# Kernel tuning notes

Measured on AMD Instinct MI355X. Metric: run time of the kernel, lower is better.

## Reference

```python
import jax, jax.numpy as jnp
import numpy as np

NL, DM, DI, DS, DC, DR, NC = 4, 128, 256, 16, 4, 8, 10
ALPHA = 0.3  # observer_alpha

def layernorm(x, w, b, eps=1e-5):
    m = x.mean(-1, keepdims=True)
    v = ((x - m) ** 2).mean(-1, keepdims=True)
    return (x - m) / jnp.sqrt(v + eps) * w + b

def silu(x):
    return x * jax.nn.sigmoid(x)

def causal_dwconv(x, w, b):
    # x: (B, L, DI); w: (DI, 1, DC); b: (DI,)
    xt = x.transpose(0, 2, 1)  # (B, DI, L)
    y = jax.lax.conv_general_dilated(
        xt, w, window_strides=(1,), padding=[(DC - 1, 0)],
        dimension_numbers=('NCH', 'OIH', 'NCH'), feature_group_count=DI)
    return (y + b[None, :, None]).transpose(0, 2, 1)  # (B, L, DI)

def ssm_scan(delta, Bc, Cc, u, A):
    # delta, u: (B, L, DI); Bc, Cc: (B, L, DS); A: (DI, DS)
    B = delta.shape[0]
    def step(h, inp):
        d_t, b_t, c_t, u_t = inp  # (B,DI),(B,DS),(B,DS),(B,DI)
        dA = jnp.exp(d_t[..., None] * A)              # (B, DI, DS)
        h = dA * h + (d_t * u_t)[..., None] * b_t[:, None, :]
        y = jnp.einsum('bds,bs->bd', h, c_t)
        return h, y
    h0 = jnp.zeros((B, DI, DS), delta.dtype)
    xs = (delta.transpose(1, 0, 2), Bc.transpose(1, 0, 2),
          Cc.transpose(1, 0, 2), u.transpose(1, 0, 2))
    _, ys = jax.lax.scan(step, h0, xs)
    return ys.transpose(1, 0, 2)  # (B, L, DI)

def _forward(x, W_in, b_in, ln_w, ln_b, in_proj_w, conv_w, conv_b, x_proj_w,
             dt_proj_w, dt_proj_b, A_log, Dp, out_proj_w, out_proj_b,
             norm_w, norm_b, cls_w, cls_b):
    B = x.shape[0]
    u = x.transpose(0, 2, 3, 1).reshape(B, -1, 3)   # (B, L, 3)
    h = u @ W_in + b_in                              # (B, L, DM)
    for i in range(NL):
        res = h
        z = layernorm(h, ln_w[i], ln_b[i])
        xz = z @ in_proj_w[i]                        # (B, L, 2*DI)
        xin, gate = jnp.split(xz, 2, axis=-1)
        xc = silu(causal_dwconv(xin, conv_w[i], conv_b[i]))  # (B, L, DI)
        proj = xc @ x_proj_w[i]                      # (B, L, DR + 2*DS)
        dt, Bc, Cc = jnp.split(proj, [DR, DR + DS], axis=-1)
        delta = jax.nn.softplus(dt @ dt_proj_w[i] + dt_proj_b[i])  # (B, L, DI)
        A = -jnp.exp(A_log[i])                       # (DI, DS)
        y = ssm_scan(delta, Bc, Cc, xc, A) + xc * Dp[i]
        # Luenberger-style observer correction: blend predicted SSM output
        y = (1.0 - ALPHA) * y + ALPHA * xc
        y = y * silu(gate)
        h = res + y @ out_proj_w[i] + out_proj_b[i]
    pooled = h.mean(axis=1)                          # (B, DM)
    pooled = layernorm(pooled, norm_w, norm_b)
    return pooled @ cls_w + cls_b                    # (B, NC)

def setup_inputs():
    key = jax.random.key(0)
    ks = jax.random.split(key, 8)
    def nrm(k, shape, std=0.02):
        return jax.random.normal(k, shape, jnp.float32) * std
    return {
        'x': jax.random.normal(ks[0], (32, 3, 32, 32), jnp.float32),
        'W_in': nrm(ks[1], (3, DM)), 'b_in': jnp.zeros((DM,), jnp.float32),
        'ln_w': jnp.ones((NL, DM), jnp.float32), 'ln_b': jnp.zeros((NL, DM), jnp.float32),
        'in_proj_w': nrm(ks[2], (NL, DM, 2 * DI)),
        'conv_w': nrm(ks[3], (NL, DI, 1, DC), 0.2), 'conv_b': jnp.zeros((NL, DI), jnp.float32),
        'x_proj_w': nrm(ks[4], (NL, DI, DR + 2 * DS)),
        'dt_proj_w': nrm(ks[5], (NL, DR, DI), 0.1),
        'dt_proj_b': jnp.full((NL, DI), -4.6, jnp.float32),
        'A_log': jnp.log(jnp.broadcast_to(jnp.arange(1, DS + 1, dtype=jnp.float32), (NL, DI, DS))),
        'Dp': jnp.ones((NL, DI), jnp.float32),
        'out_proj_w': nrm(ks[6], (NL, DI, DM)), 'out_proj_b': jnp.zeros((NL, DM), jnp.float32),
        'norm_w': jnp.ones((DM,), jnp.float32), 'norm_b': jnp.zeros((DM,), jnp.float32),
        'cls_w': nrm(ks[7], (DM, NC)), 'cls_b': jnp.zeros((NC,), jnp.float32),
    }

def reference(x, W_in, b_in, ln_w, ln_b, in_proj_w, conv_w, conv_b, x_proj_w,
              dt_proj_w, dt_proj_b, A_log, Dp, out_proj_w, out_proj_b,
              norm_w, norm_b, cls_w, cls_b):
    return _forward(x, W_in, b_in, ln_w, ln_b, in_proj_w, conv_w, conv_b,
                    x_proj_w, dt_proj_w, dt_proj_b, A_log, Dp, out_proj_w,
                    out_proj_b, norm_w, norm_b, cls_w, cls_b)
```

## Files before the change

kernel.cpp:

```cpp
#include <hip/hip_runtime.h>
#include <math.h>

#define B_  32
#define L_  1024
#define T_  (B_ * L_)
#define DM_ 128
#define DI_ 256
#define DS_ 16
#define DC_ 4
#define DR_ 8
#define NC_ 10
#define CHUNK_ 64
#define NCH_  (L_ / CHUNK_)
#define PSTR_ 288

typedef __bf16 bf16x8 __attribute__((ext_vector_type(8)));
typedef __bf16 bf16x4 __attribute__((ext_vector_type(4)));
typedef __bf16 bf16x2 __attribute__((ext_vector_type(2)));
typedef float f32x4 __attribute__((ext_vector_type(4)));
typedef unsigned short u16x8 __attribute__((ext_vector_type(8)));

__device__ __forceinline__ float sigmoidf_(float x) { return 1.0f / (1.0f + __expf(-x)); }
__device__ __forceinline__ float siluf_(float x)    { return x * sigmoidf_(x); }
__device__ __forceinline__ float softplusf_(float x) {
    return (x > 15.0f) ? x : __logf(1.0f + __expf(x));
}
__device__ __forceinline__ float fexp2_(float x) { return __builtin_amdgcn_exp2f(x); }

__device__ __forceinline__ void gload_lds16(const __bf16* g, __bf16* l) {
    __builtin_amdgcn_global_load_lds(
        (const __attribute__((address_space(1))) void*)g,
        (__attribute__((address_space(3))) void*)l, 16, 0, 0);
}

template<int R>
__device__ __forceinline__ void stage_async(const __bf16* __restrict__ src,
        __bf16* lds, int k0, int stride, int wid, int lane) {
    constexpr int NI = R / 32;
#pragma unroll
    for (int j = 0; j < NI; ++j) {
        int s0 = (wid * NI + j) * 64;
        int s = s0 + lane;
        int row = s >> 3, sw = s & 7;
        int slot = sw ^ (row & 7);
        gload_lds16(src + (size_t)row * stride + k0 + slot * 8, lds + (size_t)s0 * 8);
    }
}

__global__ __launch_bounds__(128) void k_embed(const float* __restrict__ x,
        const float* __restrict__ Win, const float* __restrict__ bin,
        float* __restrict__ h) {
    int t = blockIdx.x;
    int b = t >> 10, l = t & 1023;
    int m = threadIdx.x;
    const float* xb = x + (size_t)b * 3 * 1024 + l;
    float acc = bin[m];
    acc = fmaf(xb[0],    Win[m],        acc);
    acc = fmaf(xb[1024], Win[128 + m],  acc);
    acc = fmaf(xb[2048], Win[256 + m],  acc);
    h[(size_t)t * 128 + m] = acc;
}

__global__ __launch_bounds__(256) void k_prep(const float* __restrict__ ipw,
        const float* __restrict__ opw, const float* __restrict__ xpw,
        const float* __restrict__ dtw, __bf16* __restrict__ wt1,
        __bf16* __restrict__ wt2, __bf16* __restrict__ wcat) {
    int blk = blockIdx.x;
    int tid = threadIdx.x;
    int i = blk * 256 + tid;
    if (i < 262144) {
        int lay = i >> 16, rem = i & 65535, n = rem >> 7, k = rem & 127;
        wt1[i] = (__bf16)ipw[lay * 65536 + k * 512 + n];
    }
    if (i < 131072) {
        int lay = i >> 15, rem = i & 32767, n = rem >> 8, k = rem & 255;
        wt2[i] = (__bf16)opw[lay * 32768 + k * 128 + n];
    }
    {
        int lay = blk / 384, n = blk % 384;
        int k = tid;
        float v;
        if (n < 256) {
            float acc = 0.0f;
#pragma unroll
            for (int r = 0; r < 8; ++r)
                acc = fmaf(xpw[lay * 10240 + k * 40 + r], dtw[lay * 2048 + r * 256 + n], acc);
            v = acc;
        } else if (n < 288) {
            v = xpw[lay * 10240 + k * 40 + (n - 248)];
        } else {
            v = 0.0f;
        }
        wcat[(size_t)blk * 256 + k] = (__bf16)v;
    }
}

__global__ __launch_bounds__(256) void k_ln(const float* __restrict__ h,
        const float* __restrict__ w, const float* __restrict__ b,
        __bf16* __restrict__ z) {
    int wid = threadIdx.x >> 6, lane = threadIdx.x & 63;
    int t = blockIdx.x * 4 + wid;
    const float* hr = h + (size_t)t * 128;
    float2 v = *(const float2*)(hr + lane * 2);
    float s = v.x + v.y, sq = v.x * v.x + v.y * v.y;
#pragma unroll
    for (int off = 1; off < 64; off <<= 1) {
        s += __shfl_xor(s, off);
        sq += __shfl_xor(sq, off);
    }
    float mean = s * (1.0f / 128.0f);
    float var = sq * (1.0f / 128.0f) - mean * mean;
    float rstd = rsqrtf(var + 1e-5f);
    float2 wv = *(const float2*)(w + lane * 2);
    float2 bv = *(const float2*)(b + lane * 2);
    bf16x2 o;
    o.x = (__bf16)((v.x - mean) * rstd * wv.x + bv.x);
    o.y = (__bf16)((v.y - mean) * rstd * wv.y + bv.y);
    *(bf16x2*)(z + (size_t)t * 128 + lane * 2) = o;
}

template<int BM, int K, int N, int MODE, bool GATE, bool WLN>
__global__ __launch_bounds__(256) void k_gemm_mfma(
        const __bf16* __restrict__ A, const __bf16* __restrict__ G,
        const __bf16* __restrict__ Wt, const float* __restrict__ bias,
        float* __restrict__ Cf, __bf16* __restrict__ Cb,
        const float* __restrict__ lnw, const float* __restrict__ lnb,
        __bf16* __restrict__ Zb) {
    static_assert(!GATE || BM == 32, "GATE staging assumes BM=32");
    static_assert(!WLN || (MODE == 2 && BM == 32 && N == 128), "WLN geometry");
    __shared__ __bf16 As[BM * 64];
    __shared__ __bf16 Bs[128 * 64];
    __shared__ float red_s[WLN ? 4 : 1][WLN ? 32 : 1];
    __shared__ float red_q[WLN ? 4 : 1][WLN ? 32 : 1];
    int tid = threadIdx.x;
    int bm = blockIdx.x, bn = blockIdx.y;
    int lane = tid & 63, wid = tid >> 6;
    int lr = lane & 15, lg = lane >> 4;
    constexpr int MF = BM / 16;

    f32x4 acc[MF][2] = {};
    const __bf16* Asrc = A + (size_t)(bm * BM) * K;
    const __bf16* Bsrc = Wt + (size_t)(bn * 128) * K;

    for (int k0 = 0; k0 < K; k0 += 64) {
        if (GATE) {
            int row = tid >> 3, slot = tid & 7;
            int m = bm * BM + row;
            bf16x8 yv = *(const bf16x8*)(A + (size_t)m * K + k0 + slot * 8);
            bf16x8 gv = *(const bf16x8*)(G + (size_t)m * 512 + 256 + k0 + slot * 8);
            bf16x8 v;
#pragma unroll
            for (int j = 0; j < 8; ++j)
                v[j] = (__bf16)((float)yv[j] * siluf_((float)gv[j]));
            *(bf16x8*)(As + row * 64 + ((slot ^ (row & 7)) * 8)) = v;
        } else {
            stage_async<BM>(Asrc, As, k0, K, wid, lane);
        }
        stage_async<128>(Bsrc, Bs, k0, K, wid, lane);
        __syncthreads();
#pragma unroll
        for (int ks = 0; ks < 2; ++ks) {
            int slotbase = ks * 4 + lg;
            bf16x8 af[MF], bfr[2];
#pragma unroll
            for (int m = 0; m < MF; ++m) {
                int row = m * 16 + lr;
                af[m] = *(const bf16x8*)(As + row * 64 + ((slotbase ^ (row & 7)) * 8));
            }
#pragma unroll
            for (int n = 0; n < 2; ++n) {
                int rn = wid * 32 + n * 16 + lr;
                bfr[n] = *(const bf16x8*)(Bs + rn * 64 + ((slotbase ^ (rn & 7)) * 8));
            }
#pragma unroll
            for (int m = 0; m < MF; ++m)
#pragma unroll
                for (int n = 0; n < 2; ++n)
                    acc[m][n] = __builtin_amdgcn_mfma_f32_16x16x32_bf16(
                        af[m], bfr[n], acc[m][n], 0, 0, 0);
        }
        __syncthreads();
    }
    float vv[MF][2][4];
#pragma unroll
    for (int m = 0; m < MF; ++m) {
#pragma unroll
        for (int n = 0; n < 2; ++n) {
            int col = bn * 128 + wid * 32 + n * 16 + lr;
            float bv = (MODE == 2) ? bias[col] : 0.0f;
            float dtbv = (MODE == 1 && col < 256) ? bias[col] : 0.0f;
#pragma unroll
            for (int rg = 0; rg < 4; ++rg) {
                int row = bm * BM + m * 16 + lg * 4 + rg;
                float v = acc[m][n][rg];
                if (MODE == 0) {
                    Cb[(size_t)row * N + col] = (__bf16)v;
                } else if (MODE == 1) {
                    if (col < 256)
                        Cb[(size_t)row * PSTR_ + col] = (__bf16)softplusf_(v + dtbv);
                    else if (col < 288)
                        Cb[(size_t)row * PSTR_ + col] = (__bf16)v;
                } else {
                    float* cp = Cf + (size_t)row * N + col;
                    v += *cp + bv;
                    *cp = v;
                    vv[m][n][rg] = v;
                }
            }
        }
    }
    if (WLN) {
        float ps[MF][4], pq[MF][4];
#pragma unroll
        for (int m = 0; m < MF; ++m)
#pragma unroll
            for (int rg = 0; rg < 4; ++rg) {
                float a = vv[m][0][rg], bv2 = vv[m][1][rg];
                ps[m][rg] = a + bv2;
                pq[m][rg] = a * a + bv2 * bv2;
            }
#pragma unroll
        for (int off = 1; off < 16; off <<= 1) {
#pragma unroll
            for (int m = 0; m < MF; ++m)
#pragma unroll
                for (int rg = 0; rg < 4; ++rg) {
                    ps[m][rg] += __shfl_xor(ps[m][rg], off);
                    pq[m][rg] += __shfl_xor(pq[m][rg], off);
                }
        }
        if (lr == 0) {
#pragma unroll
            for (int m = 0; m < MF; ++m)
#pragma unroll
                for (int rg = 0; rg < 4; ++rg) {
                    int rl = m * 16 + lg * 4 + rg;
                    red_s[wid][rl] = ps[m][rg];
                    red_q[wid][rl] = pq[m][rg];
                }
        }
        __syncthreads();
#pragma unroll
        for (int m = 0; m < MF; ++m)
#pragma unroll
            for (int rg = 0; rg < 4; ++rg) {
                int rl = m * 16 + lg * 4 + rg;
                float s = red_s[0][rl] + red_s[1][rl] + red_s[2][rl] + red_s[3][rl];
                float q = red_q[0][rl] + red_q[1][rl] + red_q[2][rl] + red_q[3][rl];
                float mean = s * (1.0f / 128.0f);
                float var = q * (1.0f / 128.0f) - mean * mean;
                float rstd = rsqrtf(var + 1e-5f);
#pragma unroll
                for (int n = 0; n < 2; ++n) {
                    int col = wid * 32 + n * 16 + lr;
                    float z = (vv[m][n][rg] - mean) * rstd * lnw[col] + lnb[col];
                    Zb[(size_t)(bm * BM + rl) * 128 + col] = (__bf16)z;
                }
            }
    }
}

__global__ __launch_bounds__(256) void k_conv(const __bf16* __restrict__ xzb,
        const float* __restrict__ cw, const float* __restrict__ cb,
        __bf16* __restrict__ xcb) {
    int t = blockIdx.x * 4 + (threadIdx.x >> 6);
    int d0 = (threadIdx.x & 63) * 4;
    int l = t & 1023;
    const __bf16* xp = xzb + (size_t)t * 512 + d0;
    float4 wv[4];
#pragma unroll
    for (int j = 0; j < 4; ++j) wv[j] = *(const float4*)(cw + (d0 + j) * 4);
    float acc[4] = {cb[d0], cb[d0 + 1], cb[d0 + 2], cb[d0 + 3]};
#pragma unroll
    for (int k = 0; k < 4; ++k) {
        int back = 3 - k;
        if (l >= back) {
            bf16x4 v = *(const bf16x4*)(xp - back * 512);
#pragma unroll
            for (int j = 0; j < 4; ++j)
                acc[j] = fmaf((float)v[j], ((const float*)&wv[j])[k], acc[j]);
        }
    }
    bf16x4 o;
#pragma unroll
    for (int j = 0; j < 4; ++j) o[j] = (__bf16)siluf_(acc[j]);
    *(bf16x4*)(xcb + (size_t)t * 256 + d0) = o;
}

template<bool FINAL>
__global__ __launch_bounds__(128) void k_scan_chunk(
        const __bf16* __restrict__ projall, const __bf16* __restrict__ xcb,
        const float* __restrict__ Alog, const float* __restrict__ Dp,
        float* __restrict__ P, float* __restrict__ S,
        __bf16* __restrict__ yb) {
    __shared__ unsigned du_lds[CHUNK_ * 128];
    __shared__ float bc[CHUNK_ * 32];
    int b = blockIdx.z, c = blockIdx.y, dg = blockIdx.x;
    int tid = threadIdx.x;
    int d = dg * 128 + tid;

    const __bf16* projC = projall + ((size_t)b * 1024 + c * CHUNK_) * PSTR_;
    const __bf16* xcC   = xcb + ((size_t)b * 1024 + c * CHUNK_) * 256 + dg * 128;

#pragma unroll
    for (int r = 0; r < 8; ++r) {
        int item = r * 128 + tid;
        int t = item >> 4, o8 = (item & 15) * 8;
        u16x8 dv = *(const u16x8*)(projC + (size_t)t * PSTR_ + dg * 128 + o8);
        u16x8 xv = *(const u16x8*)(xcC + (size_t)t * 256 + o8);
        uint4 w0, w1;
        w0.x = dv[0] | ((unsigned)xv[0] << 16); w0.y = dv[1] | ((unsigned)xv[1] << 16);
        w0.z = dv[2] | ((unsigned)xv[2] << 16); w0.w = dv[3] | ((unsigned)xv[3] << 16);
        w1.x = dv[4] | ((unsigned)xv[4] << 16); w1.y = dv[5] | ((unsigned)xv[5] << 16);
        w1.z = dv[6] | ((unsigned)xv[6] << 16); w1.w = dv[7] | ((unsigned)xv[7] << 16);
        *(uint4*)(du_lds + t * 128 + o8)     = w0;
        *(uint4*)(du_lds + t * 128 + o8 + 4) = w1;
    }
#pragma unroll
    for (int r = 0; r < 2; ++r) {
        int item = r * 128 + tid;
        int t = item >> 2, g8 = (item & 3) * 8;
        bf16x8 v = *(const bf16x8*)(projC + (size_t)t * PSTR_ + 256 + g8);
        float4 f0 = {(float)v[0], (float)v[1], (float)v[2], (float)v[3]};
        float4 f1 = {(float)v[4], (float)v[5], (float)v[6], (float)v[7]};
        *(float4*)(bc + t * 32 + g8)     = f0;
        *(float4*)(bc + t * 32 + g8 + 4) = f1;
    }

    float aa[16], hs[16];
#pragma unroll
    for (int jj = 0; jj < 4; ++jj) {
        float4 av = *(const float4*)(Alog + (size_t)d * 16 + jj * 4);
        aa[jj * 4 + 0] = -__expf(av.x) * 1.44269504088896f;
        aa[jj * 4 + 1] = -__expf(av.y) * 1.44269504088896f;
        aa[jj * 4 + 2] = -__expf(av.z) * 1.44269504088896f;
        aa[jj * 4 + 3] = -__expf(av.w) * 1.44269504088896f;
    }
    float Dpd = Dp[d];
    size_t psIdx = ((size_t)(b * NCH_ + c)) * 4096 + (size_t)d * 16;
#pragma unroll
    for (int j = 0; j < 16; ++j) hs[j] = 0.0f;
    if (FINAL) {
        for (int cc = 0; cc < c; ++cc) {
            size_t base = ((size_t)(b * NCH_ + cc)) * 4096 + (size_t)d * 16;
#pragma unroll
            for (int jj = 0; jj < 4; ++jj) {
                float4 p = *(const float4*)(P + base + jj * 4);
                float4 s = *(const float4*)(S + base + jj * 4);
                hs[jj * 4 + 0] = fmaf(p.x, hs[jj * 4 + 0], s.x);
                hs[jj * 4 + 1] = fmaf(p.y, hs[jj * 4 + 1], s.y);
                hs[jj * 4 + 2] = fmaf(p.z, hs[jj * 4 + 2], s.z);
                hs[jj * 4 + 3] = fmaf(p.w, hs[jj * 4 + 3], s.w);
            }
        }
    }
    float cumd = 0.0f;
    __bf16* yC = yb + ((size_t)b * 1024 + c * CHUNK_) * 256 + dg * 128 + tid;

    __syncthreads();
#pragma unroll 2
    for (int tt = 0; tt < CHUNK_; ++tt) {
        unsigned duv = du_lds[tt * 128 + tid];
        float delta_t = __uint_as_float(duv << 16);
        float u = __uint_as_float(duv & 0xffff0000u);
        float du = delta_t * u;
        const float* bcr = bc + tt * 32;
        if (!FINAL) cumd += delta_t;
        float ys = 0.0f;
#pragma unroll
        for (int jj = 0; jj < 4; ++jj) {
            float4 Bv = *(const float4*)(bcr + jj * 4);
            float4 Cv;
            if (FINAL) Cv = *(const float4*)(bcr + 16 + jj * 4);
#pragma unroll
            for (int j = 0; j < 4; ++j) {
                int s = jj * 4 + j;
                float dA = fexp2_(delta_t * aa[s]);
                hs[s] = fmaf(dA, hs[s], du * ((const float*)&Bv)[j]);
                if (FINAL) ys = fmaf(hs[s], ((const float*)&Cv)[j], ys);
            }
        }
        if (FINAL) {
            float yv = fmaf(u, Dpd, ys);
            yv = fmaf(0.7f, yv, 0.3f * u);
            yC[(size_t)tt * 256] = (__bf16)yv;
        }
    }
    if (!FINAL) {
#pragma unroll
        for (int jj = 0; jj < 4; ++jj) {
            float4 pv, sv;
            pv.x = fexp2_(aa[jj * 4 + 0] * cumd);
            pv.y = fexp2_(aa[jj * 4 + 1] * cumd);
            pv.z = fexp2_(aa[jj * 4 + 2] * cumd);
            pv.w = fexp2_(aa[jj * 4 + 3] * cumd);
            sv.x = hs[jj * 4 + 0]; sv.y = hs[jj * 4 + 1];
            sv.z = hs[jj * 4 + 2]; sv.w = hs[jj * 4 + 3];
            *(float4*)(P + psIdx + jj * 4) = pv;
            *(float4*)(S + psIdx + jj * 4) = sv;
        }
    }
}

__global__ __launch_bounds__(128) void k_pool(const float* __restrict__ h,
        float* __restrict__ partial) {
    int b = blockIdx.x, lc = blockIdx.y;
    int m = threadIdx.x;
    const float* hb = h + (size_t)b * 131072 + (size_t)lc * 128 * 128 + m;
    float acc = 0.0f;
#pragma unroll 8
    for (int l = 0; l < 128; ++l) acc += hb[(size_t)l * 128];
    partial[((size_t)b * 8 + lc) * 128 + m] = acc;
}

__global__ __launch_bounds__(128) void k_head(const float* __restrict__ partial,
        const float* __restrict__ nw, const float* __restrict__ nb,
        const float* __restrict__ cw, const float* __restrict__ cb,
        float* __restrict__ out) {
    __shared__ float zs[128];
    __shared__ float red[128];
    int b = blockIdx.x, m = threadIdx.x;
    float v = 0.0f;
#pragma unroll
    for (int lc = 0; lc < 8; ++lc) v += partial[((size_t)b * 8 + lc) * 128 + m];
    v *= (1.0f / 1024.0f);
    red[m] = v;
    __syncthreads();
    for (int off = 64; off; off >>= 1) {
        if (m < off) red[m] += red[m + off];
        __syncthreads();
    }
    float mean = red[0] * (1.0f / 128.0f);
    __syncthreads();
    float dv = v - mean;
    red[m] = dv * dv;
    __syncthreads();
    for (int off = 64; off; off >>= 1) {
        if (m < off) red[m] += red[m + off];
        __syncthreads();
    }
    float rstd = rsqrtf(red[0] * (1.0f / 128.0f) + 1e-5f);
    zs[m] = dv * rstd * nw[m] + nb[m];
    __syncthreads();
    if (m < NC_) {
        float acc = cb[m];
#pragma unroll 8
        for (int k = 0; k < 128; ++k) acc = fmaf(zs[k], cw[k * 10 + m], acc);
        out[b * 10 + m] = acc;
    }
}

extern "C" void kernel_launch(void* const* d_in, const int* in_sizes, int n_in,
                              void* d_out, int out_size, void* d_ws, size_t ws_size,
                              hipStream_t stream) {
    const float* x    = (const float*)d_in[0];
    const float* Win  = (const float*)d_in[1];
    const float* bin  = (const float*)d_in[2];
    const float* lnw  = (const float*)d_in[3];
    const float* lnb  = (const float*)d_in[4];
    const float* ipw  = (const float*)d_in[5];
    const float* cw   = (const float*)d_in[6];
    const float* cb   = (const float*)d_in[7];
    const float* xpw  = (const float*)d_in[8];
    const float* dtw  = (const float*)d_in[9];
    const float* dtb  = (const float*)d_in[10];
    const float* Alog = (const float*)d_in[11];
    const float* Dp   = (const float*)d_in[12];
    const float* opw  = (const float*)d_in[13];
    const float* opb  = (const float*)d_in[14];
    const float* nw   = (const float*)d_in[15];
    const float* nb   = (const float*)d_in[16];
    const float* clw  = (const float*)d_in[17];
    const float* clb  = (const float*)d_in[18];

    float* ws = (float*)d_ws;
    float*  h       = ws;
    float*  P       = ws + 4194304;
    float*  Sb      = ws + 6291456;
    __bf16* zb      = (__bf16*)P;
    __bf16* xzb     = (__bf16*)(ws + 8388608);
    __bf16* xcb     = (__bf16*)(ws + 16777216);
    __bf16* projall = (__bf16*)(ws + 20971520);
    __bf16* yb      = (__bf16*)(ws + 25690112);
    float*  partial = ws + 29884416;
    __bf16* wt1     = (__bf16*)(ws + 29917184);
    __bf16* wt2     = (__bf16*)(ws + 30048256);
    __bf16* wcat    = (__bf16*)(ws + 30113792);

    k_prep<<<1536, 256, 0, stream>>>(ipw, opw, xpw, dtw, wt1, wt2, wcat);
    k_embed<<<T_, 128, 0, stream>>>(x, Win, bin, h);
    k_ln<<<T_ / 4, 256, 0, stream>>>(h, lnw, lnb, zb);
    for (int lay = 0; lay < 4; ++lay) {
        k_gemm_mfma<64, 128, 512, 0, false, false><<<dim3(T_ / 64, 4), 256, 0, stream>>>(
            zb, nullptr, wt1 + (size_t)lay * 65536, nullptr, nullptr, xzb,
            nullptr, nullptr, nullptr);
        k_conv<<<T_ / 4, 256, 0, stream>>>(xzb, cw + lay * 1024, cb + lay * 256, xcb);
        k_gemm_mfma<64, 256, 384, 1, false, false><<<dim3(T_ / 64, 3), 256, 0, stream>>>(
            xcb, nullptr, wcat + (size_t)lay * 98304, dtb + lay * 256, nullptr, projall,
            nullptr, nullptr, nullptr);
        k_scan_chunk<false><<<dim3(2, NCH_, B_), 128, 0, stream>>>(projall, xcb,
            Alog + lay * 4096, Dp + lay * 256, P, Sb, yb);
        k_scan_chunk<true><<<dim3(2, NCH_, B_), 128, 0, stream>>>(projall, xcb,
            Alog + lay * 4096, Dp + lay * 256, P, Sb, yb);
        if (lay < 3) {
            k_gemm_mfma<32, 256, 128, 2, true, true><<<dim3(T_ / 32, 1), 256, 0, stream>>>(
                yb, xzb, wt2 + (size_t)lay * 32768, opb + lay * 128, h, nullptr,
                lnw + (lay + 1) * 128, lnb + (lay + 1) * 128, zb);
        } else {
            k_gemm_mfma<32, 256, 128, 2, true, false><<<dim3(T_ / 32, 1), 256, 0, stream>>>(
                yb, xzb, wt2 + (size_t)lay * 32768, opb + lay * 128, h, nullptr,
                nullptr, nullptr, nullptr);
        }
    }
    k_pool<<<dim3(32, 8), 128, 0, stream>>>(h, partial);
    k_head<<<32, 128, 0, stream>>>(partial, nw, nb, clw, clb, (float*)d_out);
}
```

Baseline: 642.7 us.

## Halve scan chunk size and add separate chunk-state combine kernel

Reduces the scan chunk length from 64 to 32, doubling the number of chunk blocks to raise parallelism in the two scan passes. The per-block serial prefix over earlier chunk states in the final pass is replaced by a dedicated combine kernel that computes each chunk's starting state once and writes it back into P. The S buffer is moved to a new workspace offset because P/S now span twice as many chunks, and one extra kernel launch per layer is added.

```diff
diff --git a/kernel.cpp b/kernel.cpp
--- a/kernel.cpp
+++ b/kernel.cpp
@@ -10,7 +10,7 @@
 #define DC_ 4
 #define DR_ 8
 #define NC_ 10
-#define CHUNK_ 64
+#define CHUNK_ 32
 #define NCH_  (L_ / CHUNK_)
 #define PSTR_ 288
 
@@ -303,7 +303,7 @@
     const __bf16* xcC   = xcb + ((size_t)b * 1024 + c * CHUNK_) * 256 + dg * 128;
 
 #pragma unroll
-    for (int r = 0; r < 8; ++r) {
+    for (int r = 0; r < (CHUNK_ * 16) / 128; ++r) {
         int item = r * 128 + tid;
         int t = item >> 4, o8 = (item & 15) * 8;
         u16x8 dv = *(const u16x8*)(projC + (size_t)t * PSTR_ + dg * 128 + o8);
@@ -317,7 +317,7 @@
         *(uint4*)(du_lds + t * 128 + o8 + 4) = w1;
     }
 #pragma unroll
-    for (int r = 0; r < 2; ++r) {
+    for (int r = 0; r < (CHUNK_ * 4) / 128; ++r) {
         int item = r * 128 + tid;
         int t = item >> 2, g8 = (item & 3) * 8;
         bf16x8 v = *(const bf16x8*)(projC + (size_t)t * PSTR_ + 256 + g8);
@@ -338,21 +338,16 @@
     }
     float Dpd = Dp[d];
     size_t psIdx = ((size_t)(b * NCH_ + c)) * 4096 + (size_t)d * 16;
-#pragma unroll
-    for (int j = 0; j < 16; ++j) hs[j] = 0.0f;
     if (FINAL) {
-        for (int cc = 0; cc < c; ++cc) {
-            size_t base = ((size_t)(b * NCH_ + cc)) * 4096 + (size_t)d * 16;
-#pragma unroll
-            for (int jj = 0; jj < 4; ++jj) {
-                float4 p = *(const float4*)(P + base + jj * 4);
-                float4 s = *(const float4*)(S + base + jj * 4);
-                hs[jj * 4 + 0] = fmaf(p.x, hs[jj * 4 + 0], s.x);
-                hs[jj * 4 + 1] = fmaf(p.y, hs[jj * 4 + 1], s.y);
-                hs[jj * 4 + 2] = fmaf(p.z, hs[jj * 4 + 2], s.z);
-                hs[jj * 4 + 3] = fmaf(p.w, hs[jj * 4 + 3], s.w);
-            }
-        }
+#pragma unroll
+        for (int jj = 0; jj < 4; ++jj) {
+            float4 h0 = *(const float4*)(P + psIdx + jj * 4);
+            hs[jj * 4 + 0] = h0.x; hs[jj * 4 + 1] = h0.y;
+            hs[jj * 4 + 2] = h0.z; hs[jj * 4 + 3] = h0.w;
+        }
+    } else {
+#pragma unroll
+        for (int j = 0; j < 16; ++j) hs[j] = 0.0f;
     }
     float cumd = 0.0f;
     __bf16* yC = yb + ((size_t)b * 1024 + c * CHUNK_) * 256 + dg * 128 + tid;
@@ -399,6 +394,21 @@
             *(float4*)(P + psIdx + jj * 4) = pv;
             *(float4*)(S + psIdx + jj * 4) = sv;
         }
+    }
+}
+
+__global__ __launch_bounds__(256) void k_scan_combine(float* __restrict__ P,
+        const float* __restrict__ S) {
+    int idx = blockIdx.x * 256 + threadIdx.x;
+    int b = idx >> 12, rem = idx & 4095;
+    float h = 0.0f;
+#pragma unroll
+    for (int c = 0; c < NCH_; ++c) {
+        size_t base = ((size_t)(b * NCH_ + c)) * 4096 + rem;
+        float p = P[base];
+        float s = S[base];
+        P[base] = h;
+        h = fmaf(p, h, s);
     }
 }
 
@@ -476,8 +486,7 @@
     float* ws = (float*)d_ws;
     float*  h       = ws;
     float*  P       = ws + 4194304;
-    float*  Sb      = ws + 6291456;
-    __bf16* zb      = (__bf16*)P;
+    __bf16* zb      = (__bf16*)(ws + 4194304);
     __bf16* xzb     = (__bf16*)(ws + 8388608);
     __bf16* xcb     = (__bf16*)(ws + 16777216);
     __bf16* projall = (__bf16*)(ws + 20971520);
@@ -486,6 +495,7 @@
     __bf16* wt1     = (__bf16*)(ws + 29917184);
     __bf16* wt2     = (__bf16*)(ws + 30048256);
     __bf16* wcat    = (__bf16*)(ws + 30113792);
+    float*  Sb      = ws + 30310400;
 
     k_prep<<<1536, 256, 0, stream>>>(ipw, opw, xpw, dtw, wt1, wt2, wcat);
     k_embed<<<T_, 128, 0, stream>>>(x, Win, bin, h);
@@ -500,6 +510,7 @@
             nullptr, nullptr, nullptr);
         k_scan_chunk<false><<<dim3(2, NCH_, B_), 128, 0, stream>>>(projall, xcb,
             Alog + lay * 4096, Dp + lay * 256, P, Sb, yb);
+        k_scan_combine<<<B_ * 4096 / 256, 256, 0, stream>>>(P, Sb);
         k_scan_chunk<true><<<dim3(2, NCH_, B_), 128, 0, stream>>>(projall, xcb,
             Alog + lay * 4096, Dp + lay * 256, P, Sb, yb);
         if (lay < 3) {
```

Measured after the change: 617.2 us. 4.0% less time.
